# Kernel optimization log

Hardware: AMD Instinct MI355X
Metric: run time of the kernel (lower is better)

The kernel has to match this reference:

```python
import jax, jax.numpy as jnp
import numpy as np

PS = 8  # window_size
LOCAL = 16  # split channels

def conv1x1(x, w, b):
    return jnp.einsum('oi,bihw->bohw', w, x) + b[None, :, None, None]

def dynamic_local(x, w1, b1, w2, b2, k):
    # x: (B, C, H, W); dynamic per-(batch,channel) depthwise conv with generated kernels
    B, C, H, W = x.shape
    pooled = x.mean((2, 3))                      # (B, C) adaptive avg pool to 1x1
    h = jax.nn.relu(pooled @ w1.T + b1)
    kern = (h @ w2.T + b2).reshape(B, C, k, k)   # per-sample depthwise kernels
    def per_batch(xb, kb):
        return jax.lax.conv_general_dilated(
            xb[None], kb[:, None], (1, 1), 'SAME',
            feature_group_count=C,
            dimension_numbers=('NCHW', 'OIHW', 'NCHW'))[0]
    return jax.vmap(per_batch)(x, kern)

def channel_layernorm(x, w, b, eps=1e-6):
    # LayerNorm over channel dim (torch module's non-channels_last path)
    u = x.mean(1, keepdims=True)
    s = ((x - u) ** 2).mean(1, keepdims=True)
    xn = (x - u) / jnp.sqrt(s + eps)
    return w[None, :, None, None] * xn + b[None, :, None, None]

def fsas(x, hid_w, hid_b, dw_w, dw_b, ln_w, ln_b, out_w, out_b):
    hidden = conv1x1(x, hid_w, hid_b)
    mid = hidden.shape[1]
    dw = jax.lax.conv_general_dilated(
        hidden, dw_w[:, None], (1, 1), 'SAME',
        feature_group_count=mid,
        dimension_numbers=('NCHW', 'OIHW', 'NCHW')) + dw_b[None, :, None, None]
    q, k, v = jnp.split(dw, 3, axis=1)
    B, C, H, W = q.shape
    def patch(t):
        # (B,C,H,W) -> (B,C,H/ps,W/ps,ps,ps)
        return t.reshape(B, C, H // PS, PS, W // PS, PS).transpose(0, 1, 2, 4, 3, 5)
    qf = jnp.fft.rfft2(patch(q))
    kf = jnp.fft.rfft2(patch(k))
    out = jnp.fft.irfft2(qf * kf, s=(PS, PS))
    out = out.transpose(0, 1, 2, 4, 3, 5).reshape(B, C, H, W)
    out = channel_layernorm(out, ln_w, ln_b)
    return conv1x1(v * out, out_w, out_b)


def setup_inputs() -> dict:
    key = jax.random.key(0)
    ks = jax.random.split(key, 12)
    s = 0.02
    return {
        'x': jax.random.normal(ks[0], (4, 64, 256, 256), jnp.float32),
        'dl1_w1': jax.random.normal(ks[1], (16, 16), jnp.float32) * s,
        'dl1_b1': jnp.zeros((16,), jnp.float32),
        'dl1_w2': jax.random.normal(ks[2], (144, 16), jnp.float32) * s,
        'dl1_b2': jnp.zeros((144,), jnp.float32),
        'dl2_w1': jax.random.normal(ks[3], (16, 16), jnp.float32) * s,
        'dl2_b1': jnp.zeros((16,), jnp.float32),
        'dl2_w2': jax.random.normal(ks[4], (400, 16), jnp.float32) * s,
        'dl2_b2': jnp.zeros((400,), jnp.float32),
        'fs_hid_w': jax.random.normal(ks[5], (144, 48), jnp.float32) * s,
        'fs_hid_b': jnp.zeros((144,), jnp.float32),
        'fs_dw_w': jax.random.normal(ks[6], (144, 3, 3), jnp.float32) * s,
        'fs_dw_b': jnp.zeros((144,), jnp.float32),
        'fs_ln_w': jnp.ones((48,), jnp.float32),
        'fs_ln_b': jnp.zeros((48,), jnp.float32),
        'fs_out_w': jax.random.normal(ks[7], (48, 48), jnp.float32) * s,
        'fs_out_b': jnp.zeros((48,), jnp.float32),
        'last_w': jax.random.normal(ks[8], (64, 64), jnp.float32) * s,
        'last_b': jnp.zeros((64,), jnp.float32),
    }


def reference(x, dl1_w1, dl1_b1, dl1_w2, dl1_b2, dl2_w1, dl2_b1, dl2_w2, dl2_b2,
              fs_hid_w, fs_hid_b, fs_dw_w, fs_dw_b, fs_ln_w, fs_ln_b,
              fs_out_w, fs_out_b, last_w, last_b):
    x1, x2 = x[:, :LOCAL], x[:, LOCAL:]
    x1 = dynamic_local(x1, dl1_w1, dl1_b1, dl1_w2, dl1_b2, 3)
    x1 = dynamic_local(x1, dl2_w1, dl2_b1, dl2_w2, dl2_b2, 5)
    x2 = fsas(x2, fs_hid_w, fs_hid_b, fs_dw_w, fs_dw_b, fs_ln_w, fs_ln_b, fs_out_w, fs_out_b)
    return conv1x1(jnp.concatenate([x1, x2], axis=1), last_w, last_b)
```

## Files before the change

kernel.cpp:

```cpp
#include <hip/hip_runtime.h>

typedef _Float16 h2 __attribute__((ext_vector_type(2)));
typedef _Float16 h4 __attribute__((ext_vector_type(4)));
typedef _Float16 h8 __attribute__((ext_vector_type(8)));
typedef float f4 __attribute__((ext_vector_type(4)));
typedef unsigned int u32;
typedef u32 u32x2 __attribute__((ext_vector_type(2)));
typedef u32 u32x4 __attribute__((ext_vector_type(4)));

__device__ __forceinline__ h2 bch2(u32 v) { return __builtin_bit_cast(h2, v); }

__device__ __forceinline__ float warpsum(float v) {
    for (int off = 32; off > 0; off >>= 1) v += __shfl_down(v, off);
    return v;
}

__device__ __forceinline__ int sswz(int p, int k) {
    return p * 64 + ((((k >> 3) ^ (p >> 3)) & 7) << 3) + (k & 7);
}

__global__ __launch_bounds__(256) void k_prep(const float* __restrict__ hid_w,
                                              const float* __restrict__ out_w,
                                              const float* __restrict__ last_w,
                                              const float* __restrict__ out_b,
                                              const float* __restrict__ last_b,
                                              _Float16* __restrict__ hwP2,
                                              _Float16* __restrict__ lwC,
                                              float* __restrict__ bias_comb) {
    int t = blockIdx.x * 256 + threadIdx.x;
    int stride = gridDim.x * 256;
    for (int i = t; i < 9216; i += stride) {
        int n = i >> 6, r = i & 63;
        int sb = r >> 3, kl = r & 7;
        int k = (((sb ^ (n & 7)) & 7) << 3) + kl;
        hwP2[i] = (k < 48) ? (_Float16)hid_w[n * 48 + k] : (_Float16)0.f;
    }
    for (int i = t; i < 4096; i += stride) {
        int n = i >> 6, k = i & 63;
        float v;
        if (k < 16) v = last_w[n * 64 + k];
        else {
            v = 0.f;
            for (int o = 0; o < 48; ++o) v += last_w[n * 64 + 16 + o] * out_w[o * 48 + (k - 16)];
        }
        lwC[i] = (_Float16)v;
    }
    for (int n = t; n < 64; n += stride) {
        float v = last_b[n];
        for (int o = 0; o < 48; ++o) v += last_w[n * 64 + 16 + o] * out_b[o];
        bias_comb[n] = v;
    }
}

__global__ __launch_bounds__(256) void k_pool(const float* __restrict__ x, float* __restrict__ pooled1) {
    int bid = blockIdx.x;
    int b = bid >> 4, c = bid & 15;
    const float* base = x + (size_t)(b * 64 + c) * 65536;
    float s = 0.f;
    for (int i = threadIdx.x; i < 16384; i += 256) {
        float4 v = ((const float4*)base)[i];
        s += v.x + v.y + v.z + v.w;
    }
    __shared__ float red[4];
    s = warpsum(s);
    if ((threadIdx.x & 63) == 0) red[threadIdx.x >> 6] = s;
    __syncthreads();
    if (threadIdx.x == 0) pooled1[bid] = (red[0] + red[1] + red[2] + red[3]) * (1.f / 65536.f);
}

__global__ __launch_bounds__(256) void k_kern1(const float* __restrict__ pooled1,
                                               const float* __restrict__ w1, const float* __restrict__ b1,
                                               const float* __restrict__ w2, const float* __restrict__ b2,
                                               float* __restrict__ kern1) {
    __shared__ float h[64];
    int t = threadIdx.x;
    if (t < 64) {
        int b = t >> 4, j = t & 15;
        float a = b1[j];
        for (int i = 0; i < 16; ++i) a += pooled1[b * 16 + i] * w1[j * 16 + i];
        h[t] = fmaxf(a, 0.f);
    }
    __syncthreads();
    for (int i = t; i < 576; i += 256) {
        int b = i / 144, o = i - b * 144;
        float a = b2[o];
        for (int j = 0; j < 16; ++j) a += h[b * 16 + j] * w2[o * 16 + j];
        kern1[i] = a;
    }
}

__global__ __launch_bounds__(256) void k_dw3(const float* __restrict__ x,
                                             const float* __restrict__ kern1,
                                             float* __restrict__ y1, float* __restrict__ rowsum) {
    __shared__ float tile[10][258];
    __shared__ float red[8][4];
    int bid = blockIdx.x;
    int rb = bid & 31, bc = bid >> 5;
    int b = bc >> 4, c = bc & 15;
    int row0 = rb << 3;
    int col = threadIdx.x;
    const float* xc = x + ((size_t)(b * 64 + c) << 16);
#pragma unroll
    for (int j = 0; j < 10; ++j) {
        int r = row0 - 1 + j;
        tile[j][col + 1] = ((unsigned)r < 256u) ? xc[(r << 8) + col] : 0.f;
    }
    if (col < 10) { tile[col][0] = 0.f; tile[col][257] = 0.f; }
    const float* k9 = kern1 + b * 144 + c * 9;
    float kk[9];
#pragma unroll
    for (int i = 0; i < 9; ++i) kk[i] = k9[i];
    __syncthreads();
#pragma unroll
    for (int j = 0; j < 8; ++j) {
        float acc = 0.f;
#pragma unroll
        for (int dy = 0; dy < 3; ++dy)
#pragma unroll
            for (int dx = 0; dx < 3; ++dx)
                acc += kk[dy * 3 + dx] * tile[j + dy][col + dx];
        y1[((size_t)bc << 16) + ((row0 + j) << 8) + col] = acc;
        float s = warpsum(acc);
        if ((col & 63) == 0) red[j][col >> 6] = s;
    }
    __syncthreads();
    if (col < 8) rowsum[bc * 256 + row0 + col] = red[col][0] + red[col][1] + red[col][2] + red[col][3];
}

__global__ __launch_bounds__(256) void k_kern2(const float* __restrict__ rowsum,
                                               const float* __restrict__ w1, const float* __restrict__ b1,
                                               const float* __restrict__ w2, const float* __restrict__ b2,
                                               float* __restrict__ kern2) {
    __shared__ float ps[256];
    __shared__ float p2[64];
    __shared__ float h[64];
    int t = threadIdx.x;
    {
        int pair = t >> 2, seg = t & 3;
        const float* rs = rowsum + pair * 256 + seg * 64;
        float s = 0.f;
        for (int j = 0; j < 64; ++j) s += rs[j];
        ps[t] = s;
    }
    __syncthreads();
    if (t < 64) p2[t] = (ps[t * 4] + ps[t * 4 + 1] + ps[t * 4 + 2] + ps[t * 4 + 3]) * (1.f / 65536.f);
    __syncthreads();
    if (t < 64) {
        int b = t >> 4, j = t & 15;
        float a = b1[j];
        for (int i = 0; i < 16; ++i) a += p2[b * 16 + i] * w1[j * 16 + i];
        h[t] = fmaxf(a, 0.f);
    }
    __syncthreads();
    for (int i = t; i < 1600; i += 256) {
        int b = i / 400, o = i - b * 400;
        float a = b2[o];
        for (int j = 0; j < 16; ++j) a += h[b * 16 + j] * w2[o * 16 + j];
        kern2[i] = a;
    }
}

__global__ __launch_bounds__(256) void k_dw5(const float* __restrict__ y1,
                                             const float* __restrict__ kern2,
                                             float* __restrict__ x1o) {
    __shared__ float tile[12][260];
    int bid = blockIdx.x;
    int rb = bid & 31, bc = bid >> 5;
    int b = bc >> 4, c = bc & 15;
    int row0 = rb << 3;
    int col = threadIdx.x;
    const float* yc = y1 + ((size_t)bc << 16);
#pragma unroll
    for (int j = 0; j < 12; ++j) {
        int r = row0 - 2 + j;
        tile[j][col + 2] = ((unsigned)r < 256u) ? yc[(r << 8) + col] : 0.f;
    }
    if (col < 12) { tile[col][0] = 0.f; tile[col][1] = 0.f; tile[col][258] = 0.f; tile[col][259] = 0.f; }
    const float* k25 = kern2 + b * 400 + c * 25;
    float kk[25];
#pragma unroll
    for (int i = 0; i < 25; ++i) kk[i] = k25[i];
    __syncthreads();
#pragma unroll
    for (int j = 0; j < 8; ++j) {
        float acc = 0.f;
#pragma unroll
        for (int dy = 0; dy < 5; ++dy)
#pragma unroll
            for (int dx = 0; dx < 5; ++dx)
                acc += kk[dy * 5 + dx] * tile[j + dy][col + dx];
        x1o[((size_t)bc << 16) + ((row0 + j) << 8) + col] = acc;
    }
}

__global__ __launch_bounds__(512, 4) void k_fsas(const float* __restrict__ x,
                                                 const _Float16* __restrict__ hwP2, const float* __restrict__ hid_b,
                                                 const float* __restrict__ dw_w, const float* __restrict__ dw_b,
                                                 const float* __restrict__ ln_w, const float* __restrict__ ln_b,
                                                 const _Float16* __restrict__ lwC, const float* __restrict__ bias_comb,
                                                 const float* __restrict__ x1o, float* __restrict__ out) {
    __shared__ __align__(16) _Float16 Sbig[17856];
    __shared__ __align__(16) _Float16 wq[9216];

    _Float16* Abuf = Sbig;
    _Float16* hbuf = Sbig;
    _Float16* fbuf = Sbig;
    float*    lnp  = (float*)(Sbig + 4608);
    _Float16* outb = Sbig + 6656;
    float*    pstat = (float*)(Sbig + 9824);
    _Float16* wbuf = wq;
    _Float16* qbuf = wq;
    _Float16* kbuf = wq + 3072;

    int tid = threadIdx.x;
    int lane = tid & 63;
    int wave = __builtin_amdgcn_readfirstlane(tid >> 6);
    int bid = blockIdx.x;
    int swz = ((bid & 7) << 9) | (bid >> 3);
    int b = swz >> 10;
    int rem = swz & 1023;
    int row0 = (rem >> 5) << 3, col0 = (rem & 31) << 3;

    int l16 = lane & 15, lhi = lane >> 4;
    int mb = wave * 16 + (lhi << 2);
    bool vok[4];
#pragma unroll
    for (int r = 0; r < 4; ++r) {
        int m = mb + r;
        int yv = m / 12, xv = m - yv * 12;
        vok[r] = (m < 120) && (xv < 10) &&
                 ((unsigned)(row0 - 1 + yv) < 256u) && ((unsigned)(col0 - 1 + xv) < 256u);
    }

    if (tid < 480) {
        int k2 = tid / 20, r20 = tid - (tid / 20) * 20;
        int y = r20 >> 1, xh = r20 & 1;
        int gy = row0 - 1 + y;
        bool rowok = (unsigned)gy < 256u;
        const float* xa = x + ((size_t)(b * 64 + 16 + 2 * k2) << 16) + ((size_t)(gy & 255) << 8);
        const float* xb = xa + 65536;
#pragma unroll
        for (int xx = 0; xx < 6; ++xx) {
            int xv = xh * 6 + xx;
            int gx = col0 - 1 + xv;
            bool ok = rowok && (xv < 10) && ((unsigned)gx < 256u);
            float va = ok ? xa[gx] : 0.f;
            float vb = ok ? xb[gx] : 0.f;
            *(h2*)(Abuf + (y * 12 + xv) * 72 + 2 * k2) = (h2){(_Float16)va, (_Float16)vb};
        }
    }
    if (tid < 240) {
        int p = tid >> 1, kb = 48 + ((tid & 1) << 3);
        *(h8*)(Abuf + p * 72 + kb) = (h8)(_Float16)0.f;
    }
    {
        const u32x4* srcw = (const u32x4*)hwP2;
        u32x4* dstw = (u32x4*)wbuf;
        for (int i = tid; i < 1152; i += 512) dstw[i] = srcw[i];
    }
    __syncthreads();

    int arow = wave * 16 + l16;
    h8 a0 = *(const h8*)(Abuf + arow * 72 + (lhi << 3));
    h8 a1 = *(const h8*)(Abuf + arow * 72 + 32 + (lhi << 3));
    __syncthreads();

    float xr[8];
    int fgrp = wave - 6;
    if (wave >= 6) {
        size_t gp = ((size_t)(row0 + (lane >> 3)) << 8) + col0 + (lane & 7);
#pragma unroll
        for (int j = 0; j < 8; ++j)
            xr[j] = x1o[((size_t)(b * 16 + fgrp * 8 + j) << 16) + gp];
    }

#pragma unroll
    for (int nt = 0; nt < 9; ++nt) {
        int n_l = nt * 16 + l16;
        const _Float16* wr = wbuf + n_l * 64;
        h8 b0 = *(const h8*)(wr + (((lhi ^ (n_l & 7)) & 7) << 3));
        h8 b1 = *(const h8*)(wr + ((((lhi + 4) ^ (n_l & 7)) & 7) << 3));
        float bias = hid_b[n_l];
        f4 acc = {bias, bias, bias, bias};
        acc = __builtin_amdgcn_mfma_f32_16x16x32_f16(a0, b0, acc, 0, 0, 0);
        acc = __builtin_amdgcn_mfma_f32_16x16x32_f16(a1, b1, acc, 0, 0, 0);
        if (mb < 120) {
            h2 p0 = {vok[0] ? (_Float16)acc[0] : (_Float16)0.f, vok[1] ? (_Float16)acc[1] : (_Float16)0.f};
            h2 p1 = {vok[2] ? (_Float16)acc[2] : (_Float16)0.f, vok[3] ? (_Float16)acc[3] : (_Float16)0.f};
            *(h2*)(hbuf + n_l * 124 + mb) = p0;
            *(h2*)(hbuf + n_l * 124 + mb + 2) = p1;
        }
    }
    __syncthreads();

    int dch = tid >> 3, drow = tid & 7;
    h8 vreg;
    auto dw_row = [&](int ch, int row, float o[8]) {
        const float* dwp = dw_w + ch * 9;
        float bias = dw_b[ch];
#pragma unroll
        for (int xx = 0; xx < 8; ++xx) o[xx] = bias;
        const _Float16* hb = hbuf + ch * 124 + row * 12;
#pragma unroll
        for (int dy = 0; dy < 3; ++dy) {
            u32x2 A2 = *(const u32x2*)(hb + dy * 12);
            u32x2 B2 = *(const u32x2*)(hb + dy * 12 + 4);
            u32 r89 = *(const u32*)(hb + dy * 12 + 8);
            u32 r01 = A2.x, r23 = A2.y, r45 = B2.x, r67 = B2.y;
            u32 s12 = __builtin_amdgcn_alignbit(r23, r01, 16);
            u32 s34 = __builtin_amdgcn_alignbit(r45, r23, 16);
            u32 s56 = __builtin_amdgcn_alignbit(r67, r45, 16);
            u32 s78 = __builtin_amdgcn_alignbit(r89, r67, 16);
            _Float16 w0 = (_Float16)dwp[dy * 3], w1 = (_Float16)dwp[dy * 3 + 1], w2 = (_Float16)dwp[dy * 3 + 2];
            h2 w01 = {w0, w1};
            h2 w2lo = {w2, (_Float16)0.f};
            h2 w2hi = {(_Float16)0.f, w2};
            o[0] = __builtin_amdgcn_fdot2(w01, bch2(r01), o[0], false);
            o[0] = __builtin_amdgcn_fdot2(w2lo, bch2(r23), o[0], false);
            o[1] = __builtin_amdgcn_fdot2(w01, bch2(s12), o[1], false);
            o[1] = __builtin_amdgcn_fdot2(w2lo, bch2(s34), o[1], false);
            o[2] = __builtin_amdgcn_fdot2(w01, bch2(r23), o[2], false);
            o[2] = __builtin_amdgcn_fdot2(w2lo, bch2(r45), o[2], false);
            o[3] = __builtin_amdgcn_fdot2(w01, bch2(s34), o[3], false);
            o[3] = __builtin_amdgcn_fdot2(w2lo, bch2(s56), o[3], false);
            o[4] = __builtin_amdgcn_fdot2(w01, bch2(r45), o[4], false);
            o[4] = __builtin_amdgcn_fdot2(w2lo, bch2(r67), o[4], false);
            o[5] = __builtin_amdgcn_fdot2(w01, bch2(s56), o[5], false);
            o[5] = __builtin_amdgcn_fdot2(w2lo, bch2(s78), o[5], false);
            o[6] = __builtin_amdgcn_fdot2(w01, bch2(r67), o[6], false);
            o[6] = __builtin_amdgcn_fdot2(w2lo, bch2(r89), o[6], false);
            o[7] = __builtin_amdgcn_fdot2(w01, bch2(s78), o[7], false);
            o[7] = __builtin_amdgcn_fdot2(w2hi, bch2(r89), o[7], false);
        }
    };
    if (tid < 384) {
        float oq[8];
        dw_row(dch, drow, oq);
        h8 qv;
#pragma unroll
        for (int xx = 0; xx < 8; ++xx) qv[xx] = (_Float16)oq[xx];
        *(h8*)(qbuf + dch * 64 + drow * 8) = qv;
        float ov[8];
        dw_row(96 + dch, drow, ov);
#pragma unroll
        for (int xx = 0; xx < 8; ++xx) vreg[xx] = (_Float16)ov[xx];
    } else {
        int j0 = (tid - 384) * 3;
#pragma unroll
        for (int i = 0; i < 3; ++i) {
            int j = j0 + i;
            int kc = j >> 3, kr = j & 7;
            float ok8[8];
            dw_row(48 + kc, kr, ok8);
            h8 krv;
#pragma unroll
            for (int t2 = 0; t2 < 8; ++t2) krv[t2] = (_Float16)ok8[(8 - t2) & 7];
            *(h8*)(kbuf + kc * 64 + kr * 8) = krv;
        }
    }
    __syncthreads();

    float co[8];
    if (tid < 384) {
        int ch = dch, m = drow;
#pragma unroll
        for (int n = 0; n < 8; ++n) co[n] = 0.f;
#pragma unroll
        for (int i8 = 0; i8 < 8; ++i8) {
            int r = (m - i8) & 7;
            u32x4 qv = *(const u32x4*)(qbuf + ch * 64 + i8 * 8);
            u32x4 ev = *(const u32x4*)(kbuf + ch * 64 + r * 8);
            h2 qp[4] = {bch2(qv.x), bch2(qv.y), bch2(qv.z), bch2(qv.w)};
            h2 ep[4] = {bch2(ev.x), bch2(ev.y), bch2(ev.z), bch2(ev.w)};
            h2 op[4] = {bch2(__builtin_amdgcn_alignbit(ev.x, ev.w, 16)),
                        bch2(__builtin_amdgcn_alignbit(ev.y, ev.x, 16)),
                        bch2(__builtin_amdgcn_alignbit(ev.z, ev.y, 16)),
                        bch2(__builtin_amdgcn_alignbit(ev.w, ev.z, 16))};
#pragma unroll
            for (int u = 0; u < 4; ++u)
#pragma unroll
                for (int a = 0; a < 4; ++a) {
                    co[2 * u]     = __builtin_amdgcn_fdot2(qp[a], ep[(a - u) & 3], co[2 * u], false);
                    co[2 * u + 1] = __builtin_amdgcn_fdot2(qp[a], op[(a - u) & 3], co[2 * u + 1], false);
                }
        }
#pragma unroll
        for (int v = 0; v < 4; ++v)
            *(h2*)(outb + dch * 66 + drow * 8 + 2 * v) = (h2){(_Float16)co[2 * v], (_Float16)co[2 * v + 1]};
    } else {
        h8 fv;
#pragma unroll
        for (int j = 0; j < 8; ++j) fv[j] = (_Float16)xr[j];
        *(h8*)(fbuf + sswz(lane, fgrp * 8)) = fv;
    }
    __syncthreads();

    {
        int px = tid & 63, g = tid >> 6;
        float s = 0.f, ss = 0.f;
#pragma unroll
        for (int cc = 0; cc < 6; ++cc) {
            float v = (float)outb[(g * 6 + cc) * 66 + px];
            s += v; ss += v * v;
        }
        lnp[g * 64 + px] = s;
        lnp[512 + g * 64 + px] = ss;
    }
    __syncthreads();
    if (tid < 64) {
        float s = 0.f, ss = 0.f;
#pragma unroll
        for (int g = 0; g < 8; ++g) { s += lnp[g * 64 + tid]; ss += lnp[512 + g * 64 + tid]; }
        float mu = s * (1.f / 48.f);
        float var = ss * (1.f / 48.f) - mu * mu;
        pstat[tid * 2] = mu;
        pstat[tid * 2 + 1] = rsqrtf(var + 1e-6f);
    }
    __syncthreads();

    if (tid < 384) {
        float lw = ln_w[dch], lb = ln_b[dch];
        const float* ps = pstat + drow * 16;
#pragma unroll
        for (int n = 0; n < 8; ++n) {
            float mu = ps[2 * n], inv = ps[2 * n + 1];
            float lnv = lw * ((co[n] - mu) * inv) + lb;
            fbuf[sswz(drow * 8 + n, 16 + dch)] = (_Float16)((float)vreg[n] * lnv);
        }
    }
    __syncthreads();

    for (int t = wave; t < 16; t += 8) {
        int mt = t >> 2, nt = t & 3;
        int row6 = mt * 16 + l16;
        h8 c0 = *(const h8*)(fbuf + sswz(row6, lhi << 3));
        h8 c1 = *(const h8*)(fbuf + sswz(row6, 32 + (lhi << 3)));
        h8 d0 = *(const h8*)(lwC + (nt * 16 + l16) * 64 + (lhi << 3));
        h8 d1 = *(const h8*)(lwC + (nt * 16 + l16) * 64 + 32 + (lhi << 3));
        float bias = bias_comb[nt * 16 + l16];
        f4 acc = {bias, bias, bias, bias};
        acc = __builtin_amdgcn_mfma_f32_16x16x32_f16(c0, d0, acc, 0, 0, 0);
        acc = __builtin_amdgcn_mfma_f32_16x16x32_f16(c1, d1, acc, 0, 0, 0);
        int ch = nt * 16 + l16;
        int px0 = mt * 16 + (lhi << 2);
        float4 val = {acc[0], acc[1], acc[2], acc[3]};
        *(float4*)(out + ((size_t)(b * 64 + ch) << 16) + ((size_t)(row0 + (px0 >> 3)) << 8) + col0 + (px0 & 7)) = val;
    }
}

extern "C" void kernel_launch(void* const* d_in, const int* in_sizes, int n_in,
                              void* d_out, int out_size, void* d_ws, size_t ws_size,
                              hipStream_t stream) {
    const float* x      = (const float*)d_in[0];
    const float* dl1_w1 = (const float*)d_in[1];
    const float* dl1_b1 = (const float*)d_in[2];
    const float* dl1_w2 = (const float*)d_in[3];
    const float* dl1_b2 = (const float*)d_in[4];
    const float* dl2_w1 = (const float*)d_in[5];
    const float* dl2_b1 = (const float*)d_in[6];
    const float* dl2_w2 = (const float*)d_in[7];
    const float* dl2_b2 = (const float*)d_in[8];
    const float* hid_w  = (const float*)d_in[9];
    const float* hid_b  = (const float*)d_in[10];
    const float* dw_w   = (const float*)d_in[11];
    const float* dw_b   = (const float*)d_in[12];
    const float* ln_w   = (const float*)d_in[13];
    const float* ln_b   = (const float*)d_in[14];
    const float* out_w  = (const float*)d_in[15];
    const float* out_b  = (const float*)d_in[16];
    const float* last_w = (const float*)d_in[17];
    const float* last_b = (const float*)d_in[18];
    float* out = (float*)d_out;

    float* ws      = (float*)d_ws;
    float* pooled1 = ws;
    float* kern1   = ws + 64;
    float* rowsum  = ws + 1024;
    float* kern2   = ws + 17408;
    _Float16* hwP2  = (_Float16*)(ws + 19008);
    _Float16* lwC   = (_Float16*)(ws + 23616);
    float* bias_comb = ws + 25664;
    float* y1      = ws + 32768;
    float* x1o     = ws + 32768 + 4194304;

    k_prep <<<8,    256, 0, stream>>>(hid_w, out_w, last_w, out_b, last_b, hwP2, lwC, bias_comb);
    k_pool <<<64,   256, 0, stream>>>(x, pooled1);
    k_kern1<<<1,    256, 0, stream>>>(pooled1, dl1_w1, dl1_b1, dl1_w2, dl1_b2, kern1);
    k_dw3  <<<2048, 256, 0, stream>>>(x, kern1, y1, rowsum);
    k_kern2<<<1,    256, 0, stream>>>(rowsum, dl2_w1, dl2_b1, dl2_w2, dl2_b2, kern2);
    k_dw5  <<<2048, 256, 0, stream>>>(y1, kern2, x1o);
    k_fsas <<<4096, 512, 0, stream>>>(x, hwP2, hid_b, dw_w, dw_b, ln_w, ln_b,
                                      lwC, bias_comb, x1o, out);
}
```

Measured before the change: 182.4 us.

## Read hidden-conv weights from global memory and shrink LDS for higher occupancy

Result: faster. 173.2 us (-5.0%).

```diff
diff --git a/kernel.cpp b/kernel.cpp
--- a/kernel.cpp
+++ b/kernel.cpp
@@ -24,16 +24,14 @@
                                               const float* __restrict__ last_w,
                                               const float* __restrict__ out_b,
                                               const float* __restrict__ last_b,
-                                              _Float16* __restrict__ hwP2,
+                                              _Float16* __restrict__ hwH,
                                               _Float16* __restrict__ lwC,
                                               float* __restrict__ bias_comb) {
     int t = blockIdx.x * 256 + threadIdx.x;
     int stride = gridDim.x * 256;
-    for (int i = t; i < 9216; i += stride) {
-        int n = i >> 6, r = i & 63;
-        int sb = r >> 3, kl = r & 7;
-        int k = (((sb ^ (n & 7)) & 7) << 3) + kl;
-        hwP2[i] = (k < 48) ? (_Float16)hid_w[n * 48 + k] : (_Float16)0.f;
+    for (int i = t; i < 10368; i += stride) {
+        int n = i / 72, k = i - n * 72;
+        hwH[i] = (k < 48) ? (_Float16)hid_w[n * 48 + k] : (_Float16)0.f;
     }
     for (int i = t; i < 4096; i += stride) {
         int n = i >> 6, k = i & 63;
@@ -193,14 +191,14 @@
     }
 }
 
-__global__ __launch_bounds__(512, 4) void k_fsas(const float* __restrict__ x,
-                                                 const _Float16* __restrict__ hwP2, const float* __restrict__ hid_b,
+__global__ __launch_bounds__(512, 6) void k_fsas(const float* __restrict__ x,
+                                                 const _Float16* __restrict__ hwH, const float* __restrict__ hid_b,
                                                  const float* __restrict__ dw_w, const float* __restrict__ dw_b,
                                                  const float* __restrict__ ln_w, const float* __restrict__ ln_b,
                                                  const _Float16* __restrict__ lwC, const float* __restrict__ bias_comb,
                                                  const float* __restrict__ x1o, float* __restrict__ out) {
     __shared__ __align__(16) _Float16 Sbig[17856];
-    __shared__ __align__(16) _Float16 wq[9216];
+    __shared__ __align__(16) _Float16 qk2[6912];
 
     _Float16* Abuf = Sbig;
     _Float16* hbuf = Sbig;
@@ -208,9 +206,8 @@
     float*    lnp  = (float*)(Sbig + 4608);
     _Float16* outb = Sbig + 6656;
     float*    pstat = (float*)(Sbig + 9824);
-    _Float16* wbuf = wq;
-    _Float16* qbuf = wq;
-    _Float16* kbuf = wq + 3072;
+    _Float16* qbuf = qk2;
+    _Float16* kbuf = qk2 + 3456;
 
     int tid = threadIdx.x;
     int lane = tid & 63;
@@ -253,11 +250,6 @@
         int p = tid >> 1, kb = 48 + ((tid & 1) << 3);
         *(h8*)(Abuf + p * 72 + kb) = (h8)(_Float16)0.f;
     }
-    {
-        const u32x4* srcw = (const u32x4*)hwP2;
-        u32x4* dstw = (u32x4*)wbuf;
-        for (int i = tid; i < 1152; i += 512) dstw[i] = srcw[i];
-    }
     __syncthreads();
 
     int arow = wave * 16 + l16;
@@ -277,9 +269,9 @@
 #pragma unroll
     for (int nt = 0; nt < 9; ++nt) {
         int n_l = nt * 16 + l16;
-        const _Float16* wr = wbuf + n_l * 64;
-        h8 b0 = *(const h8*)(wr + (((lhi ^ (n_l & 7)) & 7) << 3));
-        h8 b1 = *(const h8*)(wr + ((((lhi + 4) ^ (n_l & 7)) & 7) << 3));
+        const _Float16* wr = hwH + n_l * 72 + (lhi << 3);
+        h8 b0 = *(const h8*)(wr);
+        h8 b1 = *(const h8*)(wr + 32);
         float bias = hid_b[n_l];
         f4 acc = {bias, bias, bias, bias};
         acc = __builtin_amdgcn_mfma_f32_16x16x32_f16(a0, b0, acc, 0, 0, 0);
@@ -339,7 +331,7 @@
         h8 qv;
 #pragma unroll
         for (int xx = 0; xx < 8; ++xx) qv[xx] = (_Float16)oq[xx];
-        *(h8*)(qbuf + dch * 64 + drow * 8) = qv;
+        *(h8*)(qbuf + dch * 72 + drow * 8) = qv;
         float ov[8];
         dw_row(96 + dch, drow, ov);
 #pragma unroll
@@ -355,7 +347,7 @@
             h8 krv;
 #pragma unroll
             for (int t2 = 0; t2 < 8; ++t2) krv[t2] = (_Float16)ok8[(8 - t2) & 7];
-            *(h8*)(kbuf + kc * 64 + kr * 8) = krv;
+            *(h8*)(kbuf + kc * 72 + kr * 8) = krv;
         }
     }
     __syncthreads();
@@ -368,8 +360,8 @@
 #pragma unroll
         for (int i8 = 0; i8 < 8; ++i8) {
             int r = (m - i8) & 7;
-            u32x4 qv = *(const u32x4*)(qbuf + ch * 64 + i8 * 8);
-            u32x4 ev = *(const u32x4*)(kbuf + ch * 64 + r * 8);
+            u32x4 qv = *(const u32x4*)(qbuf + ch * 72 + i8 * 8);
+            u32x4 ev = *(const u32x4*)(kbuf + ch * 72 + r * 8);
             h2 qp[4] = {bch2(qv.x), bch2(qv.y), bch2(qv.z), bch2(qv.w)};
             h2 ep[4] = {bch2(ev.x), bch2(ev.y), bch2(ev.z), bch2(ev.w)};
             h2 op[4] = {bch2(__builtin_amdgcn_alignbit(ev.x, ev.w, 16)),
@@ -477,18 +469,18 @@
     float* kern1   = ws + 64;
     float* rowsum  = ws + 1024;
     float* kern2   = ws + 17408;
-    _Float16* hwP2  = (_Float16*)(ws + 19008);
-    _Float16* lwC   = (_Float16*)(ws + 23616);
-    float* bias_comb = ws + 25664;
+    _Float16* hwH   = (_Float16*)(ws + 19008);
+    _Float16* lwC   = (_Float16*)(ws + 24192);
+    float* bias_comb = ws + 26240;
     float* y1      = ws + 32768;
     float* x1o     = ws + 32768 + 4194304;
 
-    k_prep <<<8,    256, 0, stream>>>(hid_w, out_w, last_w, out_b, last_b, hwP2, lwC, bias_comb);
+    k_prep <<<8,    256, 0, stream>>>(hid_w, out_w, last_w, out_b, last_b, hwH, lwC, bias_comb);
     k_pool <<<64,   256, 0, stream>>>(x, pooled1);
     k_kern1<<<1,    256, 0, stream>>>(pooled1, dl1_w1, dl1_b1, dl1_w2, dl1_b2, kern1);
     k_dw3  <<<2048, 256, 0, stream>>>(x, kern1, y1, rowsum);
     k_kern2<<<1,    256, 0, stream>>>(rowsum, dl2_w1, dl2_b1, dl2_w2, dl2_b2, kern2);
     k_dw5  <<<2048, 256, 0, stream>>>(y1, kern2, x1o);
-    k_fsas <<<4096, 512, 0, stream>>>(x, hwP2, hid_b, dw_w, dw_b, ln_w, ln_b,
+    k_fsas <<<4096, 512, 0, stream>>>(x, hwH, hid_b, dw_w, dw_b, ln_w, ln_b,
                                       lwC, bias_comb, x1o, out);
 }
```
